# Optimization experiments

Hardware: AMD Instinct MI355X
Metric: run time of the kernel (lower is better)

Reference implementation:

```python
import jax, jax.numpy as jnp
import numpy as np
jax.config.update("jax_enable_x64", True)

SR = 44100
STATE_SIZE = 4096
RG0, R10, C10, C20 = 1.0e6, 4.7e5, 3.3e-9, 1.0e-9

# Reconstructed DK-method incidence matrices (3 circuit nodes, 1 vsrc):
#   Vin at node1; C1 node1->node2; R1 node2->gnd; pot top node2->node3;
#   pot bottom node3->gnd; C2 node3->gnd; output at node3 (pot wiper).
_Nu = np.array([[1., 0., 0.]])
_Nx = np.array([[1., -1., 0.], [0., 0., 1.]])
_Nr = np.array([[0., 1., 0.]])
_Nv = np.array([[0., 1., -1.], [0., 0., 1.]])
_No = np.array([[0., 0., 1.]])


def _preamp_forward(x, cond, state, alpha_rg, alpha_r1, alpha_c1, alpha_c2, cond_w, cond_b):
    f64 = jnp.float64
    T = 1.0 / SR
    Nu, Nx, Nr, Nv, No = (jnp.asarray(m, f64) for m in (_Nu, _Nx, _Nr, _Nv, _No))
    Zm = jnp.eye(2, dtype=f64)
    n_nodes, n_vsrc = 3, 1
    zpad = jnp.zeros((2, n_vsrc), f64)
    Nvp = jnp.concatenate([Nv, zpad], axis=1)                      # [2,4]
    Nxp = jnp.concatenate([Nx, zpad], axis=1)                      # [2,4]
    Nop = jnp.concatenate([No, jnp.zeros((1, n_vsrc), f64)], 1)    # [1,4]
    Nup = jnp.concatenate([jnp.zeros((n_nodes, n_vsrc), f64), jnp.eye(n_vsrc, dtype=f64)], 0)  # [4,1]

    # component updates (sigmoid-trimmed around nominal values)
    RG = (0.9 + jax.nn.sigmoid(alpha_rg[0]).astype(f64) * 0.2) * RG0
    R1 = (0.99 + jax.nn.sigmoid(alpha_r1[0]).astype(f64) * 0.02) * R10
    C1 = (0.9 + jax.nn.sigmoid(alpha_c1[0]).astype(f64) * 0.2) * C10
    C2 = (0.9 + jax.nn.sigmoid(alpha_c2[0]).astype(f64) * 0.2) * C20
    Gr = jnp.reshape(1.0 / R1, (1, 1))
    Gx = jnp.diag(jnp.stack([2.0 * C1 / T, 2.0 * C2 / T]))

    # cond block: affine -> sigmoid -> log pot taper
    pot = jax.nn.sigmoid(cond[:, 0] * cond_w[0] + cond_b[0])
    p = jnp.clip((jnp.power(10.0, pot) - 1.0) / 9.0, 1e-4, 1.0 - 1e-4).astype(f64)  # [B]

    # state-space update
    top = jnp.concatenate([Nr.T @ Gr @ Nr + Nx.T @ Gx @ Nx, Nu.T], axis=1)
    bot = jnp.concatenate([Nu, jnp.zeros((n_vsrc, n_vsrc), f64)], axis=1)
    So_inv = jnp.linalg.inv(jnp.concatenate([top, bot], axis=0))   # [4,4]
    Q = Nvp @ So_inv @ Nvp.T                                        # [2,2]
    Ux = Nxp @ So_inv @ Nvp.T                                       # [2,2]
    Uo = Nop @ So_inv @ Nvp.T                                       # [1,2]
    Uu = Nup.T @ So_inv @ Nvp.T                                     # [1,2]
    ZGx = 2.0 * Zm @ Gx
    Ao = ZGx @ Nxp @ So_inv @ Nxp.T - Zm
    Bo = ZGx @ Nxp @ So_inv @ Nup
    Do = Nop @ So_inv @ Nxp.T
    Eo = Nop @ So_inv @ Nup

    d = jnp.stack([(1.0 - p) * RG, p * RG], axis=-1)                # [B,2]
    Rv = d[:, :, None] * jnp.eye(2, dtype=f64)                      # [B,2,2] diag
    RvQ = jnp.linalg.inv(Rv + Q)                                    # [B,2,2]

    ZGxUx = ZGx @ Ux
    A = Ao - ZGxUx @ RvQ @ Ux.T                                     # [B,2,2]
    Bm = Bo - ZGxUx @ RvQ @ Uu.T                                    # [B,2,1]
    Dm = Do - Uo @ RvQ @ Ux.T                                       # [B,1,2]
    Em = Eo - Uo @ RvQ @ Uu.T                                       # [B,1,1]

    # quadratic characteristic poly [1, -tr, det] (= real part of prod(z-eig))
    def poly2(M):
        tr = M[..., 0, 0] + M[..., 1, 1]
        det = M[..., 0, 0] * M[..., 1, 1] - M[..., 0, 1] * M[..., 1, 0]
        return jnp.stack([jnp.ones_like(tr), -tr, det], axis=-1)    # [B,3]

    den = poly2(A)
    num = poly2(A - Bm @ Dm) + (Em[:, 0] - 1.0) * den

    nb = 1 + STATE_SIZE // 2
    z = jnp.exp(-1j * jnp.linspace(0.0, jnp.pi, nb))                # complex128 [nb]

    def polyval(c):  # Horner, highest degree first
        c = c.astype(jnp.complex128)
        return (c[:, 0, None] * z + c[:, 1, None]) * z + c[:, 2, None]  # [B,nb]

    h = polyval(num) / polyval(den)                                 # [B,nb]

    L = x.shape[1]
    st = jnp.concatenate([state[:, L:, :], x], axis=1).astype(f64)  # [B,S,1]
    sf = jnp.fft.rfft(st, axis=1)                                   # [B,nb,1]
    out = jnp.fft.irfft(sf * h[:, :, None], axis=1).astype(jnp.float32)
    return out[:, -L:, :]


def setup_inputs() -> dict:
    key = jax.random.key(0)
    k0, k1, k2 = jax.random.split(key, 3)
    B, L = 2048, 2048
    return {
        "x": jax.random.normal(k0, (B, L, 1), dtype=jnp.float32),
        "cond": jax.random.uniform(k1, (B, 1), dtype=jnp.float32),
        "state": jax.random.normal(k2, (B, STATE_SIZE, 1), dtype=jnp.float32) * 0.1,
        "alpha_rg": jnp.zeros((1,), jnp.float32),
        "alpha_r1": jnp.zeros((1,), jnp.float32),
        "alpha_c1": jnp.zeros((1,), jnp.float32),
        "alpha_c2": jnp.zeros((1,), jnp.float32),
        "cond_w": jnp.ones((1,), jnp.float32),
        "cond_b": jnp.zeros((1,), jnp.float32),
    }


def reference(x, cond, state, alpha_rg, alpha_r1, alpha_c1, alpha_c2, cond_w, cond_b):
    return _preamp_forward(x, cond, state, alpha_rg, alpha_r1, alpha_c1, alpha_c2, cond_w, cond_b)
```

## Files before the change

kernel.cpp:

```cpp
#include <hip/hip_runtime.h>
#include <math.h>

#define NFFT 4096
#define HALF 2048
#define LSEG 2048
#define SSZ 4096

typedef float v2f __attribute__((ext_vector_type(2)));


static __device__ __forceinline__ v2f cmul(v2f a, v2f b) {
    return (v2f){ fmaf(-a.y, b.y, a.x * b.x), fmaf(a.y, b.x, a.x * b.y) };
}

static __device__ __forceinline__ int PAD(int i) { return i + (i >> 4); }

template <int SGN>
static __device__ __forceinline__ void dft16(v2f r[16]) {
    const float S = (float)SGN;
    v2f t[16];
#pragma unroll
    for (int n1 = 0; n1 < 4; ++n1) {
        v2f a = r[n1], b = r[n1 + 4], c = r[n1 + 8], d = r[n1 + 12];
        v2f A = a + c, B = b + d, C = a - c, D = b - d;
        v2f iD = (v2f){ -S * D.y, S * D.x };
        t[n1 * 4 + 0] = A + B;
        t[n1 * 4 + 1] = C + iD;
        t[n1 * 4 + 2] = A - B;
        t[n1 * 4 + 3] = C - iD;
    }
    const float CC[10] = {1.f, 0.92387953251f, 0.70710678119f, 0.38268343236f, 0.f,
                          -0.38268343236f, -0.70710678119f, -0.92387953251f, -1.f, -0.92387953251f};
    const float SS[10] = {0.f, 0.38268343236f, 0.70710678119f, 0.92387953251f, 1.f,
                          0.92387953251f, 0.70710678119f, 0.38268343236f, 0.f, -0.38268343236f};
#pragma unroll
    for (int n1 = 1; n1 < 4; ++n1) {
#pragma unroll
        for (int m2 = 1; m2 < 4; ++m2) {
            const int k = n1 * m2;
            t[n1 * 4 + m2] = cmul(t[n1 * 4 + m2], (v2f){CC[k], S * SS[k]});
        }
    }
#pragma unroll
    for (int m2 = 0; m2 < 4; ++m2) {
        v2f a = t[m2], b = t[4 + m2], c = t[8 + m2], d = t[12 + m2];
        v2f A = a + c, B = b + d, C = a - c, D = b - d;
        v2f iD = (v2f){ -S * D.y, S * D.x };
        r[m2]      = A + B;
        r[m2 + 4]  = C + iD;
        r[m2 + 8]  = A - B;
        r[m2 + 12] = C - iD;
    }
}

static __device__ __forceinline__ void twiddle_chain(v2f r[16], v2f w1) {
    v2f w2 = cmul(w1, w1);
    v2f w3 = cmul(w2, w1);
    v2f w4 = cmul(w2, w2);
    v2f w5 = cmul(w4, w1);
    v2f w6 = cmul(w4, w2);
    v2f w7 = cmul(w4, w3);
    v2f w8 = cmul(w4, w4);
    r[1] = cmul(r[1], w1);   r[2] = cmul(r[2], w2);
    r[3] = cmul(r[3], w3);   r[4] = cmul(r[4], w4);
    r[5] = cmul(r[5], w5);   r[6] = cmul(r[6], w6);
    r[7] = cmul(r[7], w7);   r[8] = cmul(r[8], w8);
    r[9]  = cmul(r[9],  cmul(w8, w1));
    r[10] = cmul(r[10], cmul(w8, w2));
    r[11] = cmul(r[11], cmul(w8, w3));
    r[12] = cmul(r[12], cmul(w8, w4));
    r[13] = cmul(r[13], cmul(w8, w5));
    r[14] = cmul(r[14], cmul(w8, w6));
    r[15] = cmul(r[15], cmul(w8, w7));
}

__global__ __launch_bounds__(256)
void preamp_fft_kernel(const float* __restrict__ x,
                       const float* __restrict__ state,
                       const float* __restrict__ cond,
                       const float* __restrict__ a_rg,
                       const float* __restrict__ a_r1,
                       const float* __restrict__ a_c1,
                       const float* __restrict__ a_c2,
                       const float* __restrict__ cond_w,
                       const float* __restrict__ cond_b,
                       float* __restrict__ out, int B) {
    __shared__ v2f a_s[NFFT + NFFT / 16];
    __shared__ float cf[10];

    const int t = threadIdx.x;
    const int b0 = 2 * blockIdx.x;
    const int b1 = (b0 + 1 < B) ? b0 + 1 : b0;

    const float* st0 = state + (size_t)b0 * SSZ + (SSZ - LSEG);
    const float* xb0 = x + (size_t)b0 * LSEG;
    const float* st1 = state + (size_t)b1 * SSZ + (SSZ - LSEG);
    const float* xb1 = x + (size_t)b1 * LSEG;

    for (int i = t; i < NFFT; i += 256) {
        float fa, fb;
        if (i < LSEG) { fa = st0[i]; fb = st1[i]; }
        else          { fa = xb0[i - LSEG]; fb = xb1[i - LSEG]; }
        a_s[PAD(i)] = (v2f){fa, fb};
    }

    if ((t & 127) == 0) {
        const int who = t >> 7;
        const int bb = who ? b1 : b0;

        const double RG = (0.9 + (double)(1.0f / (1.0f + expf(-a_rg[0]))) * 0.2) * 1.0e6;
        const double R1 = (0.99 + (double)(1.0f / (1.0f + expf(-a_r1[0]))) * 0.02) * 4.7e5;
        const double C1 = (0.9 + (double)(1.0f / (1.0f + expf(-a_c1[0]))) * 0.2) * 3.3e-9;
        const double C2 = (0.9 + (double)(1.0f / (1.0f + expf(-a_c2[0]))) * 0.2) * 1.0e-9;
        const double g1 = 1.0 / R1;
        const double gc1 = 2.0 * C1 * 44100.0;
        const double gc2 = 2.0 * C2 * 44100.0;

        float zf = cond[bb] * cond_w[0] + cond_b[0];
        float pot = 1.0f / (1.0f + expf(-zf));
        float prf = (powf(10.0f, pot) - 1.0f) / 9.0f;
        prf = fminf(fmaxf(prf, 1e-4f), 1.0f - 1e-4f);
        const double p = (double)prf;

        const double ds = gc1 + g1;
        double S[4][4] = {
            {0.0, 0.0,        0.0,       1.0},
            {0.0, 1.0 / ds,   0.0,       gc1 / ds},
            {0.0, 0.0,        1.0 / gc2, 0.0},
            {1.0, gc1 / ds,   0.0,       -gc1 * g1 / ds}};

        double Q00 = S[1][1] - S[1][2] - S[2][1] + S[2][2];
        double Q01 = S[1][2] - S[2][2];
        double Q10 = S[2][1] - S[2][2];
        double Q11 = S[2][2];

        double Ux00 = S[0][1] - S[0][2] - S[1][1] + S[1][2];
        double Ux01 = S[0][2] - S[1][2];
        double Ux10 = S[2][1] - S[2][2];
        double Ux11 = S[2][2];

        double Uo0 = S[2][1] - S[2][2], Uo1 = S[2][2];
        double Uu0 = S[3][1] - S[3][2], Uu1 = S[3][2];

        double P00 = S[0][0] - S[0][1] - S[1][0] + S[1][1];
        double P01 = S[0][2] - S[1][2];
        double P10 = S[2][0] - S[2][1];
        double P11 = S[2][2];

        double Ao00 = 2.0 * gc1 * P00 - 1.0, Ao01 = 2.0 * gc1 * P01;
        double Ao10 = 2.0 * gc2 * P10,       Ao11 = 2.0 * gc2 * P11 - 1.0;

        double Bo0 = 2.0 * gc1 * (S[0][3] - S[1][3]);
        double Bo1 = 2.0 * gc2 * S[2][3];

        double Do0 = S[2][0] - S[2][1], Do1 = S[2][2];
        double Eo  = S[2][3];

        double T00 = 2.0 * gc1 * Ux00, T01 = 2.0 * gc1 * Ux01;
        double T10 = 2.0 * gc2 * Ux10, T11 = 2.0 * gc2 * Ux11;

        double d0 = (1.0 - p) * RG, d1v = p * RG;
        double M00 = d0 + Q00, M01 = Q01, M10 = Q10, M11 = d1v + Q11;
        double idet = 1.0 / (M00 * M11 - M01 * M10);
        double G00 =  M11 * idet, G01 = -M01 * idet;
        double G10 = -M10 * idet, G11 =  M00 * idet;

        double TG00 = T00 * G00 + T01 * G10, TG01 = T00 * G01 + T01 * G11;
        double TG10 = T10 * G00 + T11 * G10, TG11 = T10 * G01 + T11 * G11;

        double A00 = Ao00 - (TG00 * Ux00 + TG01 * Ux01);
        double A01 = Ao01 - (TG00 * Ux10 + TG01 * Ux11);
        double A10 = Ao10 - (TG10 * Ux00 + TG11 * Ux01);
        double A11 = Ao11 - (TG10 * Ux10 + TG11 * Ux11);

        double Bm0 = Bo0 - (TG00 * Uu0 + TG01 * Uu1);
        double Bm1 = Bo1 - (TG10 * Uu0 + TG11 * Uu1);

        double w0v = Uo0 * G00 + Uo1 * G10, w1v = Uo0 * G01 + Uo1 * G11;
        double Dm0 = Do0 - (w0v * Ux00 + w1v * Ux01);
        double Dm1 = Do1 - (w0v * Ux10 + w1v * Ux11);
        double Em  = Eo  - (w0v * Uu0 + w1v * Uu1);

        double den1 = -(A00 + A11);
        double den2 = A00 * A11 - A01 * A10;
        double Mm00 = A00 - Bm0 * Dm0, Mm01 = A01 - Bm0 * Dm1;
        double Mm10 = A10 - Bm1 * Dm0, Mm11 = A11 - Bm1 * Dm1;
        double num0 = Em;
        double num1 = -(Mm00 + Mm11) + (Em - 1.0) * den1;
        double num2 = (Mm00 * Mm11 - Mm01 * Mm10) + (Em - 1.0) * den2;

        cf[who * 5 + 0] = (float)num0;
        cf[who * 5 + 1] = (float)num1;
        cf[who * 5 + 2] = (float)(num0 + num1 + num2);
        cf[who * 5 + 3] = (float)den1;
        cf[who * 5 + 4] = (float)(1.0 + den1 + den2);
    }
    __syncthreads();

    const float TW4096 = 0.00153398078788564f;
    const float TW256  = 0.02454369260617026f;
    const float HW4096 = 0.00076699039394282f;

    v2f r[16];

#pragma unroll
    for (int m = 0; m < 16; ++m) r[m] = a_s[PAD(t + 256 * m)];
    dft16<-1>(r);
    {
        float sw, cw;
        __sincosf((float)t * TW4096, &sw, &cw);
        twiddle_chain(r, (v2f){cw, -sw});
    }
#pragma unroll
    for (int m = 0; m < 16; ++m) a_s[PAD(t + 256 * m)] = r[m];
    __syncthreads();

    {
        const int sub = t >> 4, j = t & 15;
        const int base = sub * 256 + j;
#pragma unroll
        for (int m = 0; m < 16; ++m) r[m] = a_s[PAD(base + 16 * m)];
        dft16<-1>(r);
        float sw, cw;
        __sincosf((float)j * TW256, &sw, &cw);
        twiddle_chain(r, (v2f){cw, -sw});
#pragma unroll
        for (int m = 0; m < 16; ++m) a_s[PAD(base + 16 * m)] = r[m];
    }
    __syncthreads();

    {
        const int base = 16 * t;
#pragma unroll
        for (int m = 0; m < 16; ++m) r[m] = a_s[PAD(base + m)];
        dft16<-1>(r);
        const int klo = ((t & 15) << 4) | (t >> 4);
        __syncthreads();
#pragma unroll
        for (int m = 0; m < 16; ++m) a_s[PAD((m << 8) | klo)] = r[m];
    }
    __syncthreads();

    {
        const float an0 = cf[0], an1 = cf[1], asn = cf[2], ad1 = cf[3], asd = cf[4];
        const float bn0 = cf[5], bn1 = cf[6], bsn = cf[7], bd1 = cf[8], bsd = cf[9];

        for (int i = t; i <= HALF; i += 256) {
            const int k  = i;
            const int kr = (NFFT - i) & (NFFT - 1);
            v2f Wk = a_s[PAD(k)];
            v2f Wr = a_s[PAD(kr)];
            float Xar = 0.5f * (Wk.x + Wr.x), Xai = 0.5f * (Wk.y - Wr.y);
            float Xbr = 0.5f * (Wk.y + Wr.y), Xbi = 0.5f * (Wr.x - Wk.x);
            float sh, ch;
            __sincosf((float)k * HW4096, &sh, &ch);
            float m2s = -2.0f * sh;
            float ur = m2s * sh, ui = m2s * ch;
            float pr = ur + 2.0f;
            float tar = an0 * pr + an1, tai = an0 * ui;
            float nr = asn + ur * tar - ui * tai, ni = ur * tai + ui * tar;
            float tbr = pr + ad1;
            float dr = asd + ur * tbr - ui * ui, di = ur * ui + ui * tbr;
            float inv = __builtin_amdgcn_rcpf(dr * dr + di * di);
            float Har = (nr * dr + ni * di) * inv, Hai = (ni * dr - nr * di) * inv;
            tar = bn0 * pr + bn1; tai = bn0 * ui;
            nr = bsn + ur * tar - ui * tai; ni = ur * tai + ui * tar;
            tbr = pr + bd1;
            dr = bsd + ur * tbr - ui * ui; di = ur * ui + ui * tbr;
            inv = __builtin_amdgcn_rcpf(dr * dr + di * di);
            float Hbr = (nr * dr + ni * di) * inv, Hbi = (ni * dr - nr * di) * inv;

            float Yar = Har * Xar - Hai * Xai, Yai = Har * Xai + Hai * Xar;
            float Ybr = Hbr * Xbr - Hbi * Xbi, Ybi = Hbr * Xbi + Hbi * Xbr;
            a_s[PAD(k)] = (v2f){Yar - Ybi, Yai + Ybr};
            if (kr != k) a_s[PAD(kr)] = (v2f){Yar + Ybi, Ybr - Yai};
        }
    }
    __syncthreads();

    {
        const int base = 16 * t;
        const int klo = ((t & 15) << 4) | (t >> 4);
#pragma unroll
        for (int m = 0; m < 16; ++m) r[m] = a_s[PAD((m << 8) | klo)];
        dft16<1>(r);
        __syncthreads();
#pragma unroll
        for (int m = 0; m < 16; ++m) a_s[PAD(base + m)] = r[m];
    }
    __syncthreads();

    {
        const int sub = t >> 4, j = t & 15;
        const int base = sub * 256 + j;
#pragma unroll
        for (int m = 0; m < 16; ++m) r[m] = a_s[PAD(base + 16 * m)];
        float sw, cw;
        __sincosf((float)j * TW256, &sw, &cw);
        twiddle_chain(r, (v2f){cw, sw});
        dft16<1>(r);
#pragma unroll
        for (int m = 0; m < 16; ++m) a_s[PAD(base + 16 * m)] = r[m];
    }
    __syncthreads();

    {
#pragma unroll
        for (int m = 0; m < 16; ++m) r[m] = a_s[PAD(t + 256 * m)];
        float sw, cw;
        __sincosf((float)t * TW4096, &sw, &cw);
        twiddle_chain(r, (v2f){cw, sw});
        dft16<1>(r);
        const float scale = 1.0f / (float)NFFT;
        float* ob0 = out + (size_t)b0 * LSEG;
        float* ob1 = out + (size_t)b1 * LSEG;
#pragma unroll
        for (int m = 8; m < 16; ++m) {
            const int idx = t + 256 * (m - 8);
            float ya = r[m].x * scale;
            float yb = (b1 != b0) ? r[m].y * scale : ya;
            ob0[idx] = ya;
            ob1[idx] = yb;
        }
    }
}

extern "C" void kernel_launch(void* const* d_in, const int* in_sizes, int n_in,
                              void* d_out, int out_size, void* d_ws, size_t ws_size,
                              hipStream_t stream) {
    const float* x     = (const float*)d_in[0];
    const float* cond  = (const float*)d_in[1];
    const float* state = (const float*)d_in[2];
    const float* a_rg  = (const float*)d_in[3];
    const float* a_r1  = (const float*)d_in[4];
    const float* a_c1  = (const float*)d_in[5];
    const float* a_c2  = (const float*)d_in[6];
    const float* c_w   = (const float*)d_in[7];
    const float* c_b   = (const float*)d_in[8];
    float* out = (float*)d_out;

    const int B = in_sizes[1];

    preamp_fft_kernel<<<dim3((B + 1) / 2), dim3(256), 0, stream>>>(
        x, state, cond, a_rg, a_r1, a_c1, a_c2, c_w, c_b, out, B);
}
```

Before: 121.2 us.

## Use packed-FP32 inline asm for complex math and vectorize input loads

Replaces the complex multiply and the ±i rotations in the radix-16 butterflies with inline v_pk_mul/v_pk_fma/v_pk_add asm using op_sel and neg modifiers, which removes explicit swizzle and negate instructions. It also rewrites the global-to-LDS load as unrolled 128-bit vector loads, four samples per thread per iteration, and adds a min-blocks hint of 4 to __launch_bounds__. The inline asm limits compiler scheduling, and the occupancy hint may force register spills.

```diff
diff --git a/kernel.cpp b/kernel.cpp
--- a/kernel.cpp
+++ b/kernel.cpp
@@ -7,32 +7,54 @@
 #define SSZ 4096
 
 typedef float v2f __attribute__((ext_vector_type(2)));
-
+typedef float v4f __attribute__((ext_vector_type(4)));
 
 static __device__ __forceinline__ v2f cmul(v2f a, v2f b) {
-    return (v2f){ fmaf(-a.y, b.y, a.x * b.x), fmaf(a.y, b.x, a.x * b.y) };
+    v2f r;
+    asm("v_pk_mul_f32 %0, %1, %2 op_sel:[0,0] op_sel_hi:[0,1]\n\t"
+        "v_pk_fma_f32 %0, %1, %2, %0 op_sel:[1,1,0] op_sel_hi:[1,0,1] neg_lo:[1,0,0]"
+        : "=&v"(r) : "v"(a), "v"(b));
+    return r;
+}
+
+static __device__ __forceinline__ v2f cadd_mi(v2f c, v2f d) {
+    v2f r;
+    asm("v_pk_add_f32 %0, %1, %2 op_sel:[0,1] op_sel_hi:[1,0] neg_hi:[0,1]"
+        : "=v"(r) : "v"(c), "v"(d));
+    return r;
+}
+
+static __device__ __forceinline__ v2f cadd_pi(v2f c, v2f d) {
+    v2f r;
+    asm("v_pk_add_f32 %0, %1, %2 op_sel:[0,1] op_sel_hi:[1,0] neg_lo:[0,1]"
+        : "=v"(r) : "v"(c), "v"(d));
+    return r;
 }
 
 static __device__ __forceinline__ int PAD(int i) { return i + (i >> 4); }
 
 template <int SGN>
 static __device__ __forceinline__ void dft16(v2f r[16]) {
-    const float S = (float)SGN;
     v2f t[16];
 #pragma unroll
     for (int n1 = 0; n1 < 4; ++n1) {
         v2f a = r[n1], b = r[n1 + 4], c = r[n1 + 8], d = r[n1 + 12];
         v2f A = a + c, B = b + d, C = a - c, D = b - d;
-        v2f iD = (v2f){ -S * D.y, S * D.x };
         t[n1 * 4 + 0] = A + B;
-        t[n1 * 4 + 1] = C + iD;
         t[n1 * 4 + 2] = A - B;
-        t[n1 * 4 + 3] = C - iD;
+        if (SGN < 0) {
+            t[n1 * 4 + 1] = cadd_mi(C, D);
+            t[n1 * 4 + 3] = cadd_pi(C, D);
+        } else {
+            t[n1 * 4 + 1] = cadd_pi(C, D);
+            t[n1 * 4 + 3] = cadd_mi(C, D);
+        }
     }
     const float CC[10] = {1.f, 0.92387953251f, 0.70710678119f, 0.38268343236f, 0.f,
                           -0.38268343236f, -0.70710678119f, -0.92387953251f, -1.f, -0.92387953251f};
     const float SS[10] = {0.f, 0.38268343236f, 0.70710678119f, 0.92387953251f, 1.f,
                           0.92387953251f, 0.70710678119f, 0.38268343236f, 0.f, -0.38268343236f};
+    const float S = (float)SGN;
 #pragma unroll
     for (int n1 = 1; n1 < 4; ++n1) {
 #pragma unroll
@@ -45,11 +67,15 @@
     for (int m2 = 0; m2 < 4; ++m2) {
         v2f a = t[m2], b = t[4 + m2], c = t[8 + m2], d = t[12 + m2];
         v2f A = a + c, B = b + d, C = a - c, D = b - d;
-        v2f iD = (v2f){ -S * D.y, S * D.x };
-        r[m2]      = A + B;
-        r[m2 + 4]  = C + iD;
-        r[m2 + 8]  = A - B;
-        r[m2 + 12] = C - iD;
+        r[m2]     = A + B;
+        r[m2 + 8] = A - B;
+        if (SGN < 0) {
+            r[m2 + 4]  = cadd_mi(C, D);
+            r[m2 + 12] = cadd_pi(C, D);
+        } else {
+            r[m2 + 4]  = cadd_pi(C, D);
+            r[m2 + 12] = cadd_mi(C, D);
+        }
     }
 }
 
@@ -74,7 +100,7 @@
     r[15] = cmul(r[15], cmul(w8, w7));
 }
 
-__global__ __launch_bounds__(256)
+__global__ __launch_bounds__(256, 4)
 void preamp_fft_kernel(const float* __restrict__ x,
                        const float* __restrict__ state,
                        const float* __restrict__ cond,
@@ -97,11 +123,22 @@
     const float* st1 = state + (size_t)b1 * SSZ + (SSZ - LSEG);
     const float* xb1 = x + (size_t)b1 * LSEG;
 
-    for (int i = t; i < NFFT; i += 256) {
-        float fa, fb;
-        if (i < LSEG) { fa = st0[i]; fb = st1[i]; }
-        else          { fa = xb0[i - LSEG]; fb = xb1[i - LSEG]; }
-        a_s[PAD(i)] = (v2f){fa, fb};
+#pragma unroll
+    for (int q = 0; q < 4; ++q) {
+        const int i0 = (t + 256 * q) << 2;
+        v4f fa, fb;
+        if (q < 2) {
+            fa = *(const v4f*)(st0 + i0);
+            fb = *(const v4f*)(st1 + i0);
+        } else {
+            fa = *(const v4f*)(xb0 + (i0 - LSEG));
+            fb = *(const v4f*)(xb1 + (i0 - LSEG));
+        }
+        const int p = PAD(i0);
+        a_s[p + 0] = (v2f){fa.x, fb.x};
+        a_s[p + 1] = (v2f){fa.y, fb.y};
+        a_s[p + 2] = (v2f){fa.z, fb.z};
+        a_s[p + 3] = (v2f){fa.w, fb.w};
     }
 
     if ((t & 127) == 0) {
```

New measurement: 116.5 us. 1.04x faster.
